# Performance work log

Measured on AMD Instinct MI355X. Metric: run time of the kernel, lower is better.

## Reference

```python
import jax, jax.numpy as jnp
import numpy as np

N, E, D, L = 50000, 640000, 128, 3  # nodes, edges, channels, layers
EPS = 1e-5


def setup_inputs() -> dict:
    key = jax.random.key(0)
    ks = jax.random.split(key, 10)
    s = 1.0 / np.sqrt(D)
    inp = {
        "x": jax.random.normal(ks[0], (N, D), dtype=jnp.float32),
        "edge_attr": jax.random.normal(ks[1], (E, D), dtype=jnp.float32),
        "w_self": jax.random.normal(ks[2], (L, D, D), dtype=jnp.float32) * s,
        "b_self": jnp.zeros((L, D), dtype=jnp.float32),
        "w_in": jax.random.normal(ks[3], (L, D, D), dtype=jnp.float32) * s,
        "b_in": jnp.zeros((L, D), dtype=jnp.float32),
        "w_rel": jax.random.normal(ks[4], (L, D, D), dtype=jnp.float32) * s,
        "b_rel": jnp.zeros((L, D), dtype=jnp.float32),
        "bn_gamma": jnp.ones((L - 1, D), dtype=jnp.float32),
        "bn_beta": jnp.zeros((L - 1, D), dtype=jnp.float32),
        "edge_index": jax.random.randint(ks[5], (2, E), 0, N, dtype=jnp.int64),
    }
    return inp


def _batchnorm(h, gamma, beta):
    mu = jnp.mean(h, axis=0)
    var = jnp.mean(jnp.square(h - mu), axis=0)  # biased var (torch BN training)
    return (h - mu) * jax.lax.rsqrt(var + EPS) * gamma + beta


def reference(x, edge_attr, w_self, b_self, w_in, b_in, w_rel, b_rel,
              bn_gamma, bn_beta, edge_index):
    src, dst = edge_index[0], edge_index[1]
    # per-node in-degree for mean aggregation (zero-degree nodes -> 0)
    cnt = jax.ops.segment_sum(jnp.ones((E, 1), x.dtype), dst, num_segments=N)
    denom = jnp.maximum(cnt, 1.0)
    for i in range(L):
        # message: lin_in(x_j * edge_attr)
        msg = jnp.einsum('ed,fd->ef', x[src] * edge_attr, w_in[i]) + b_in[i]
        agg = jax.ops.segment_sum(msg, dst, num_segments=N) / denom  # scatter-mean
        x = agg + jnp.einsum('nd,fd->nf', x, w_self[i]) + b_self[i]
        edge_attr = jnp.einsum('ed,fd->ef', edge_attr, w_rel[i]) + b_rel[i]
        if i < L - 1:
            x = jax.nn.relu(_batchnorm(x, bn_gamma[i], bn_beta[i]))
            # dropout p=0.0 -> identity
    return (x, edge_attr)
```

## Files before the change

kernel.cpp:

```cpp
#include <hip/hip_runtime.h>

#define DD 128

typedef __attribute__((ext_vector_type(8))) short bf16x8;
typedef __attribute__((ext_vector_type(4))) short bf16x4;
typedef __attribute__((ext_vector_type(4))) float f32x4;
typedef unsigned short u16;

__device__ __forceinline__ unsigned short f2bf(float f) {
  union { float f; unsigned u; } v; v.f = f;
  unsigned u = v.u;
  return (unsigned short)((u + 0x7FFFu + ((u >> 16) & 1u)) >> 16);
}
__device__ __forceinline__ float bf2f(unsigned short h) {
  union { unsigned u; float f; } v; v.u = ((unsigned)h) << 16; return v.f;
}
__device__ __forceinline__ bf16x8 pack8(f32x4 a, f32x4 b) {
  bf16x8 r;
  r[0] = (short)f2bf(a.x); r[1] = (short)f2bf(a.y);
  r[2] = (short)f2bf(a.z); r[3] = (short)f2bf(a.w);
  r[4] = (short)f2bf(b.x); r[5] = (short)f2bf(b.y);
  r[6] = (short)f2bf(b.z); r[7] = (short)f2bf(b.w);
  return r;
}

__device__ __forceinline__ bool idx_is64(const int* p) {
  return (p[1] | p[3] | p[5] | p[7]) == 0;
}
__device__ __forceinline__ int ld_idx(const int* p, long long i, bool is64) {
  return is64 ? (int)((const long long*)p)[i] : p[i];
}

__global__ void k_count(const int* __restrict__ idx, int* __restrict__ cnt, int E) {
  int e = blockIdx.x * blockDim.x + threadIdx.x;
  if (e >= E) return;
  bool is64 = idx_is64(idx);
  int d = ld_idx(idx, (long long)E + e, is64);
  atomicAdd(&cnt[d], 1);
}

__global__ __launch_bounds__(1024) void k_scan(const int* __restrict__ cnt,
    int* __restrict__ row_start, int* __restrict__ cursor, int N) {
  __shared__ int part[1024];
  int t = threadIdx.x;
  int chunk = (N + 1023) >> 10;
  int lo = t * chunk, hi = lo + chunk; if (hi > N) hi = N; if (lo > N) lo = N;
  int s = 0;
  for (int i = lo; i < hi; ++i) s += cnt[i];
  part[t] = s;
  __syncthreads();
  for (int off = 1; off < 1024; off <<= 1) {
    int v = (t >= off) ? part[t - off] : 0;
    __syncthreads();
    part[t] += v;
    __syncthreads();
  }
  int run = (t == 0) ? 0 : part[t - 1];
  for (int i = lo; i < hi; ++i) {
    row_start[i] = run; cursor[i] = run; run += cnt[i];
  }
  if (t == 1023) row_start[N] = part[1023];
}

__global__ void k_fill(const int* __restrict__ idx, int* __restrict__ cursor,
                       int* __restrict__ edge_of, int* __restrict__ src_csr, int E) {
  int e = blockIdx.x * blockDim.x + threadIdx.x;
  if (e >= E) return;
  bool is64 = idx_is64(idx);
  int s = ld_idx(idx, e, is64);
  int d = ld_idx(idx, (long long)E + e, is64);
  int pos = atomicAdd(&cursor[d], 1);
  edge_of[pos] = e;
  src_csr[pos] = s;
}

template <int MODE>
__global__ __launch_bounds__(256) void k_msg(
    const float* __restrict__ x0, const u16* __restrict__ xp,
    const float* __restrict__ ea0, const u16* __restrict__ eain,
    u16* __restrict__ m, u16* __restrict__ eaC,
    const int* __restrict__ edge_of, const int* __restrict__ src_csr, int E) {
  int i = blockIdx.x * 256 + threadIdx.x;
  int k = i >> 4, c = i & 15;
  if (k >= E) return;
  int sn = src_csr[k];
  int co = c * 8;
  bf16x8 mm;
  if constexpr (MODE == 0) {
    int e = edge_of[k];
    const float* ep = ea0 + (size_t)e * DD + co;
    const float* xq = x0 + (size_t)sn * DD + co;
    f32x4 e0 = *(const f32x4*)ep, e1 = *(const f32x4*)(ep + 4);
    f32x4 xv0 = *(const f32x4*)xq, xv1 = *(const f32x4*)(xq + 4);
    *(bf16x8*)(eaC + (size_t)k * DD + co) = pack8(e0, e1);
    f32x4 p0 = e0 * xv0, p1 = e1 * xv1;
    mm = pack8(p0, p1);
  } else {
    bf16x8 ev = *(const bf16x8*)(eain + (size_t)k * DD + co);
    bf16x8 xv = *(const bf16x8*)(xp + (size_t)sn * DD + co);
#pragma unroll
    for (int j = 0; j < 8; ++j)
      mm[j] = (short)f2bf(bf2f((u16)ev[j]) * bf2f((u16)xv[j]));
  }
  *(bf16x8*)(m + (size_t)k * DD + co) = mm;
}

__global__ __launch_bounds__(256) void k_segsum(const u16* __restrict__ m,
    const int* __restrict__ row_start, u16* __restrict__ agg, int N) {
  int n = blockIdx.x * 4 + (threadIdx.x >> 6);
  if (n >= N) return;
  int lane = threadIdx.x & 63;
  int e4 = lane >> 4, c = lane & 15, co = c * 8;
  int s0 = row_start[n], s1 = row_start[n + 1];
  int len = s1 - s0;
  float acc[8];
#pragma unroll
  for (int j = 0; j < 8; ++j) acc[j] = 0.f;
  for (int kk = e4; kk < len; kk += 4) {
    bf16x8 mv = *(const bf16x8*)(m + (size_t)(s0 + kk) * DD + co);
#pragma unroll
    for (int j = 0; j < 8; ++j) acc[j] += bf2f((u16)mv[j]);
  }
#pragma unroll
  for (int j = 0; j < 8; ++j) {
    float s = acc[j];
    s += __shfl_xor(s, 16);
    s += __shfl_xor(s, 32);
    acc[j] = s;
  }
  if (e4 == 0) {
    float inv = (len > 0) ? 1.0f / (float)len : 0.0f;
    f32x4 lo, hi;
#pragma unroll
    for (int j = 0; j < 4; ++j) { lo[j] = acc[j] * inv; hi[j] = acc[4 + j] * inv; }
    *(bf16x8*)(agg + (size_t)n * DD + co) = pack8(lo, hi);
  }
}

template <bool SCATTER, typename TO>
__global__ __launch_bounds__(256, 3) void k_rel(const u16* __restrict__ ea_in,
    TO* __restrict__ ea_out, const int* __restrict__ edge_of,
    const float* __restrict__ W, const float* __restrict__ bias, int ntiles) {
  __shared__ short Wl[16384];
  for (int q = threadIdx.x; q < 4096; q += 256) {
    int off = q * 4;
    int f = off >> 7, d = off & 127;
    f32x4 w = *(const f32x4*)(W + off);
    unsigned byte = ((unsigned)(f * 256 + d * 2)) ^ (unsigned)((f & 7) << 4);
    bf16x4 s4;
    s4[0] = (short)f2bf(w.x); s4[1] = (short)f2bf(w.y);
    s4[2] = (short)f2bf(w.z); s4[3] = (short)f2bf(w.w);
    *(bf16x4*)((char*)Wl + byte) = s4;
  }
  __syncthreads();
  int wave = threadIdx.x >> 6, lane = threadIdx.x & 63;
  int r = lane & 15, g = lane >> 4;
  int tile = blockIdx.x * 4 + wave;
  if (tile >= ntiles) return;
  const u16* rowp = ea_in + (size_t)(tile * 16 + r) * DD;
  bf16x8 a8[4];
#pragma unroll
  for (int ks = 0; ks < 4; ++ks) a8[ks] = *(const bf16x8*)(rowp + ks * 32 + g * 8);
  f32x4 acc[8];
#pragma unroll
  for (int ct = 0; ct < 8; ++ct) acc[ct] = (f32x4){0.f, 0.f, 0.f, 0.f};
#pragma unroll
  for (int ct = 0; ct < 8; ++ct) {
    int f = ct * 16 + r;
    unsigned base = (unsigned)(f * 256);
    unsigned sw = (unsigned)((f & 7) << 4);
#pragma unroll
    for (int ks = 0; ks < 4; ++ks) {
      unsigned byte = (base + (unsigned)(ks * 64 + g * 16)) ^ sw;
      bf16x8 bb = *(const bf16x8*)((const char*)Wl + byte);
      acc[ct] = __builtin_amdgcn_mfma_f32_16x16x32_bf16(a8[ks], bb, acc[ct], 0, 0, 0);
    }
  }
  size_t orow[4];
#pragma unroll
  for (int j = 0; j < 4; ++j) {
    int kr = tile * 16 + g * 4 + j;
    orow[j] = SCATTER ? (size_t)edge_of[kr] : (size_t)kr;
  }
#pragma unroll
  for (int ct = 0; ct < 8; ++ct) {
    int col = ct * 16 + r;
    float bv = bias[col];
#pragma unroll
    for (int j = 0; j < 4; ++j) {
      float v = acc[ct][j] + bv;
      if constexpr (sizeof(TO) == 2) ea_out[orow[j] * DD + col] = (TO)f2bf(v);
      else                            ea_out[orow[j] * DD + col] = (TO)v;
    }
  }
}

template <typename TX, typename TO, bool STATS>
__global__ __launch_bounds__(256, 2) void k_node(const u16* __restrict__ agg,
    const TX* __restrict__ xc, const float* __restrict__ W_in,
    const float* __restrict__ W_self, const float* __restrict__ b_in,
    const float* __restrict__ b_self, const int* __restrict__ row_start,
    TO* __restrict__ xn, float* __restrict__ gsum, float* __restrict__ gssq,
    int ntiles) {
  __shared__ short Wl[DD * 256];
  for (int q = threadIdx.x; q < DD * 256 / 4; q += 256) {
    int off = q * 4;
    int f = off >> 8, k = off & 255;
    f32x4 w = (k < 128) ? *(const f32x4*)(W_in + f * 128 + k)
                        : *(const f32x4*)(W_self + f * 128 + (k - 128));
    unsigned byte = ((unsigned)(f * 512 + k * 2)) ^ (unsigned)((f & 7) << 4);
    bf16x4 s4;
    s4[0] = (short)f2bf(w.x); s4[1] = (short)f2bf(w.y);
    s4[2] = (short)f2bf(w.z); s4[3] = (short)f2bf(w.w);
    *(bf16x4*)((char*)Wl + byte) = s4;
  }
  __syncthreads();
  int wave = threadIdx.x >> 6, lane = threadIdx.x & 63;
  int tile = blockIdx.x * 4 + wave;
  if (tile >= ntiles) return;
  int r = lane & 15, g = lane >> 4;
  int arowi = tile * 16 + r;
  const u16* arow = agg + (size_t)arowi * DD;
  const TX* xrow = xc + (size_t)arowi * DD;
  bf16x8 a[8];
#pragma unroll
  for (int ks = 0; ks < 4; ++ks) a[ks] = *(const bf16x8*)(arow + ks * 32 + g * 8);
#pragma unroll
  for (int ks = 0; ks < 4; ++ks) {
    int c0 = ks * 32 + g * 8;
    if constexpr (sizeof(TX) == 2) {
      a[4 + ks] = *(const bf16x8*)(xrow + c0);
    } else {
      const float* p = (const float*)xrow + c0;
      a[4 + ks] = pack8(*(const f32x4*)p, *(const f32x4*)(p + 4));
    }
  }
  f32x4 acc[8];
#pragma unroll
  for (int ct = 0; ct < 8; ++ct) acc[ct] = (f32x4){0.f, 0.f, 0.f, 0.f};
#pragma unroll
  for (int ct = 0; ct < 8; ++ct) {
    int f = ct * 16 + r;
    unsigned base = (unsigned)(f * 512);
    unsigned sw = (unsigned)((f & 7) << 4);
#pragma unroll
    for (int ks = 0; ks < 8; ++ks) {
      unsigned byte = (base + (unsigned)(ks * 64 + g * 16)) ^ sw;
      bf16x8 b = *(const bf16x8*)((const char*)Wl + byte);
      acc[ct] = __builtin_amdgcn_mfma_f32_16x16x32_bf16(a[ks], b, acc[ct], 0, 0, 0);
    }
  }
  int nbase = tile * 16;
  float degmask[4];
#pragma unroll
  for (int j = 0; j < 4; ++j) {
    int nn = nbase + g * 4 + j;
    degmask[j] = (row_start[nn + 1] > row_start[nn]) ? 1.0f : 0.0f;
  }
#pragma unroll
  for (int ct = 0; ct < 8; ++ct) {
    int col = ct * 16 + r;
    float bi = b_in[col], bs = b_self[col];
    float s = 0.f, s2 = 0.f;
#pragma unroll
    for (int j = 0; j < 4; ++j) {
      float v = acc[ct][j] + bs + bi * degmask[j];
      if constexpr (sizeof(TO) == 2) xn[(size_t)(nbase + g * 4 + j) * DD + col] = (TO)f2bf(v);
      else                            xn[(size_t)(nbase + g * 4 + j) * DD + col] = (TO)v;
      s += v; s2 += v * v;
    }
    if constexpr (STATS) {
      s += __shfl_xor(s, 16);  s += __shfl_xor(s, 32);
      s2 += __shfl_xor(s2, 16); s2 += __shfl_xor(s2, 32);
      if (g == 0) { atomicAdd(&gsum[col], s); atomicAdd(&gssq[col], s2); }
    }
  }
}

__global__ void k_bnfin(float* __restrict__ gsum, float* __restrict__ gssq,
    const float* __restrict__ gamma, const float* __restrict__ beta,
    float* __restrict__ scale, float* __restrict__ shift, int N) {
  int d = threadIdx.x;
  float mu = gsum[d] / (float)N;
  float var = gssq[d] / (float)N - mu * mu;
  float rs = rsqrtf(var + 1e-5f);
  float sc = rs * gamma[d];
  scale[d] = sc;
  shift[d] = beta[d] - mu * sc;
  gsum[d] = 0.f;
  gssq[d] = 0.f;
}

__global__ void k_bnapply(const u16* __restrict__ xb, u16* __restrict__ xpost,
                          const float* __restrict__ scale,
                          const float* __restrict__ shift, int total8) {
  int i = blockIdx.x * blockDim.x + threadIdx.x;
  if (i >= total8) return;
  bf16x8 v = ((const bf16x8*)xb)[i];
  int c0 = (i * 8) & 127;
  bf16x8 o;
#pragma unroll
  for (int j = 0; j < 8; ++j) {
    float f = fmaxf(bf2f((u16)v[j]) * scale[c0 + j] + shift[c0 + j], 0.f);
    o[j] = (short)f2bf(f);
  }
  ((bf16x8*)xpost)[i] = o;
}

static inline size_t alignup(size_t v, size_t a) { return (v + a - 1) & ~(a - 1); }

extern "C" void kernel_launch(void* const* d_in, const int* in_sizes, int n_in,
                              void* d_out, int out_size, void* d_ws, size_t ws_size,
                              hipStream_t stream) {
  const float* x0     = (const float*)d_in[0];
  const float* ea0    = (const float*)d_in[1];
  const float* w_self = (const float*)d_in[2];
  const float* b_self = (const float*)d_in[3];
  const float* w_in   = (const float*)d_in[4];
  const float* b_in   = (const float*)d_in[5];
  const float* w_rel  = (const float*)d_in[6];
  const float* b_rel  = (const float*)d_in[7];
  const float* gamma  = (const float*)d_in[8];
  const float* beta   = (const float*)d_in[9];
  const int*   idx    = (const int*)d_in[10];

  const int N = in_sizes[0] / DD;
  const int E = in_sizes[1] / DD;

  char* w = (char*)d_ws;
  size_t off = 0;
  int* cnt       = (int*)(w + off); off = alignup(off + (size_t)N * 4, 256);
  int* row_start = (int*)(w + off); off = alignup(off + (size_t)(N + 1) * 4, 256);
  int* cursor    = (int*)(w + off); off = alignup(off + (size_t)N * 4, 256);
  int* edge_of   = (int*)(w + off); off = alignup(off + (size_t)E * 4, 256);
  int* src_csr   = (int*)(w + off); off = alignup(off + (size_t)E * 4, 256);
  float* gstats  = (float*)(w + off); off = alignup(off + 256 * 4, 256);
  float* scale   = (float*)(w + off); off = alignup(off + 128 * 4, 256);
  float* shift   = (float*)(w + off); off = alignup(off + 128 * 4, 256);
  u16* agg       = (u16*)(w + off); off = alignup(off + (size_t)N * DD * 2, 256);
  u16* xbA       = (u16*)(w + off); off = alignup(off + (size_t)N * DD * 2, 256);
  u16* xpost     = (u16*)(w + off); off = alignup(off + (size_t)N * DD * 2, 256);
  u16* eaC       = (u16*)(w + off); off = alignup(off + (size_t)E * DD * 2, 256);
  u16* mbuf      = (u16*)(w + off); off = alignup(off + (size_t)E * DD * 2, 256);
  float* gsum = gstats, *gssq = gstats + 128;
  (void)ws_size; (void)n_in; (void)out_size;

  float* out_x  = (float*)d_out;
  float* out_ea = out_x + (size_t)N * DD;

  (void)hipMemsetAsync(cnt, 0, (size_t)N * 4, stream);
  int ethreads = 256, eblocks = (E + ethreads - 1) / ethreads;
  k_count<<<eblocks, ethreads, 0, stream>>>(idx, cnt, E);
  k_scan<<<1, 1024, 0, stream>>>(cnt, row_start, cursor, N);
  k_fill<<<eblocks, ethreads, 0, stream>>>(idx, cursor, edge_of, src_csr, E);
  (void)hipMemsetAsync(gstats, 0, 256 * 4, stream);

  const int ntN = N / 16;
  const int ntE = E / 16;
  const int msgBlocks = (E * 16 + 255) / 256;
  const int segBlocks = (N + 3) / 4;
  const int relBlocks = (ntE + 3) / 4;
  const int nodeBlocks = (ntN + 3) / 4;
  const int bnBlocks = ((size_t)N * DD / 8 + 255) / 256;

  k_msg<0><<<msgBlocks, 256, 0, stream>>>(x0, nullptr, ea0, nullptr,
      mbuf, eaC, edge_of, src_csr, E);
  k_rel<false, u16><<<relBlocks, 256, 0, stream>>>(eaC, eaC, edge_of,
      w_rel, b_rel, ntE);
  k_segsum<<<segBlocks, 256, 0, stream>>>(mbuf, row_start, agg, N);
  k_node<float, u16, true><<<nodeBlocks, 256, 0, stream>>>(agg, x0,
      w_in, w_self, b_in, b_self, row_start, xbA, gsum, gssq, ntN);
  k_bnfin<<<1, 128, 0, stream>>>(gsum, gssq, gamma, beta, scale, shift, N);
  k_bnapply<<<bnBlocks, 256, 0, stream>>>(xbA, xpost, scale, shift, N * DD / 8);

  k_msg<1><<<msgBlocks, 256, 0, stream>>>(nullptr, xpost, nullptr, eaC,
      mbuf, nullptr, edge_of, src_csr, E);
  k_rel<false, u16><<<relBlocks, 256, 0, stream>>>(eaC, eaC, edge_of,
      w_rel + DD * DD, b_rel + DD, ntE);
  k_segsum<<<segBlocks, 256, 0, stream>>>(mbuf, row_start, agg, N);
  k_node<u16, u16, true><<<nodeBlocks, 256, 0, stream>>>(agg, xpost,
      w_in + DD * DD, w_self + DD * DD, b_in + DD, b_self + DD,
      row_start, xbA, gsum, gssq, ntN);
  k_bnfin<<<1, 128, 0, stream>>>(gsum, gssq, gamma + DD, beta + DD, scale, shift, N);
  k_bnapply<<<bnBlocks, 256, 0, stream>>>(xbA, xpost, scale, shift, N * DD / 8);

  k_msg<1><<<msgBlocks, 256, 0, stream>>>(nullptr, xpost, nullptr, eaC,
      mbuf, nullptr, edge_of, src_csr, E);
  k_rel<true, float><<<relBlocks, 256, 0, stream>>>(eaC, out_ea, edge_of,
      w_rel + 2 * DD * DD, b_rel + 2 * DD, ntE);
  k_segsum<<<segBlocks, 256, 0, stream>>>(mbuf, row_start, agg, N);
  k_node<u16, float, false><<<nodeBlocks, 256, 0, stream>>>(agg, xpost,
      w_in + 2 * DD * DD, w_self + 2 * DD * DD, b_in + 2 * DD, b_self + 2 * DD,
      row_start, out_x, gsum, gssq, ntN);
}
```

Measured before the change: 1.215 ms.

## Fuse message, edge-linear and batchnorm-apply into combined edge and node kernels

Merges the per-edge message kernel and the edge relation GEMM into one k_relmsg kernel, so each edge tile reads edge_attr once and writes both the message and the transformed edge features. It also drops the separate batchnorm-apply pass by applying scale, shift and ReLU on the fly when the message and node kernels read node features. This removes several full passes over E×D and N×D buffers and some kernel launches. In exchange, it double-buffers edge features because input and output rows no longer align within one kernel, it adds register pressure (launch bound 2 instead of 3), and BN+ReLU is now recomputed on every gathered source row.

```diff
diff --git a/kernel.cpp b/kernel.cpp
--- a/kernel.cpp
+++ b/kernel.cpp
@@ -75,34 +75,128 @@
 }
 
 template <int MODE>
-__global__ __launch_bounds__(256) void k_msg(
-    const float* __restrict__ x0, const u16* __restrict__ xp,
+__global__ __launch_bounds__(256, 2) void k_relmsg(
+    const float* __restrict__ x0, const u16* __restrict__ xbin,
     const float* __restrict__ ea0, const u16* __restrict__ eain,
-    u16* __restrict__ m, u16* __restrict__ eaC,
-    const int* __restrict__ edge_of, const int* __restrict__ src_csr, int E) {
-  int i = blockIdx.x * 256 + threadIdx.x;
-  int k = i >> 4, c = i & 15;
-  if (k >= E) return;
-  int sn = src_csr[k];
-  int co = c * 8;
-  bf16x8 mm;
+    u16* __restrict__ eabout, float* __restrict__ eafout,
+    u16* __restrict__ m,
+    const int* __restrict__ edge_of, const int* __restrict__ src_csr,
+    const float* __restrict__ w_rel, const float* __restrict__ b_rel,
+    const float* __restrict__ scale, const float* __restrict__ shift,
+    int ntE) {
+  __shared__ short Wl[16384];
+  for (int q = threadIdx.x; q < 4096; q += 256) {
+    int off = q * 4;
+    int f = off >> 7, d = off & 127;
+    f32x4 w = *(const f32x4*)(w_rel + off);
+    unsigned byte = ((unsigned)(f * 256 + d * 2)) ^ (unsigned)((f & 7) << 4);
+    bf16x4 s4;
+    s4[0] = (short)f2bf(w.x); s4[1] = (short)f2bf(w.y);
+    s4[2] = (short)f2bf(w.z); s4[3] = (short)f2bf(w.w);
+    *(bf16x4*)((char*)Wl + byte) = s4;
+  }
+  __syncthreads();
+  int wave = threadIdx.x >> 6, lane = threadIdx.x & 63;
+  int tile = blockIdx.x * 4 + wave;
+  if (tile >= ntE) return;
+  int r = lane & 15, g = lane >> 4;
+  int k0 = tile * 16;
+  int pos = r;
+  int co = pos * 8;
+
+  bf16x8 a8[4];
   if constexpr (MODE == 0) {
-    int e = edge_of[k];
-    const float* ep = ea0 + (size_t)e * DD + co;
-    const float* xq = x0 + (size_t)sn * DD + co;
-    f32x4 e0 = *(const f32x4*)ep, e1 = *(const f32x4*)(ep + 4);
-    f32x4 xv0 = *(const f32x4*)xq, xv1 = *(const f32x4*)(xq + 4);
-    *(bf16x8*)(eaC + (size_t)k * DD + co) = pack8(e0, e1);
-    f32x4 p0 = e0 * xv0, p1 = e1 * xv1;
-    mm = pack8(p0, p1);
+    int er = edge_of[k0 + r];
+    const float* rp = ea0 + (size_t)er * DD;
+#pragma unroll
+    for (int ks = 0; ks < 4; ++ks) {
+      const float* p = rp + ks * 32 + g * 8;
+      a8[ks] = pack8(*(const f32x4*)p, *(const f32x4*)(p + 4));
+    }
   } else {
-    bf16x8 ev = *(const bf16x8*)(eain + (size_t)k * DD + co);
-    bf16x8 xv = *(const bf16x8*)(xp + (size_t)sn * DD + co);
-#pragma unroll
-    for (int j = 0; j < 8; ++j)
-      mm[j] = (short)f2bf(bf2f((u16)ev[j]) * bf2f((u16)xv[j]));
-  }
-  *(bf16x8*)(m + (size_t)k * DD + co) = mm;
+    const u16* rp = eain + (size_t)(k0 + r) * DD;
+#pragma unroll
+    for (int ks = 0; ks < 4; ++ks) a8[ks] = *(const bf16x8*)(rp + ks * 32 + g * 8);
+  }
+
+  int kk[4], sn[4];
+#pragma unroll
+  for (int i = 0; i < 4; ++i) { kk[i] = k0 + g + 4 * i; sn[i] = src_csr[kk[i]]; }
+  f32x4 xf0[4], xf1[4], ef0[4], ef1[4];
+  bf16x8 xb[4], eb[4];
+  if constexpr (MODE == 0) {
+#pragma unroll
+    for (int i = 0; i < 4; ++i) {
+      int ei = edge_of[kk[i]];
+      const float* xp = x0 + (size_t)sn[i] * DD + co;
+      const float* ep = ea0 + (size_t)ei * DD + co;
+      xf0[i] = *(const f32x4*)xp; xf1[i] = *(const f32x4*)(xp + 4);
+      ef0[i] = *(const f32x4*)ep; ef1[i] = *(const f32x4*)(ep + 4);
+    }
+  } else {
+#pragma unroll
+    for (int i = 0; i < 4; ++i) {
+      xb[i] = *(const bf16x8*)(xbin + (size_t)sn[i] * DD + co);
+      eb[i] = *(const bf16x8*)(eain + (size_t)kk[i] * DD + co);
+    }
+  }
+  float sc[8], sh[8];
+  if constexpr (MODE >= 1) {
+    f32x4 s0 = *(const f32x4*)(scale + co), s1 = *(const f32x4*)(scale + co + 4);
+    f32x4 h0 = *(const f32x4*)(shift + co), h1 = *(const f32x4*)(shift + co + 4);
+#pragma unroll
+    for (int j = 0; j < 4; ++j) { sc[j] = s0[j]; sc[4 + j] = s1[j]; sh[j] = h0[j]; sh[4 + j] = h1[j]; }
+  }
+
+  f32x4 acc[8];
+#pragma unroll
+  for (int ct = 0; ct < 8; ++ct) acc[ct] = (f32x4){0.f, 0.f, 0.f, 0.f};
+#pragma unroll
+  for (int ct = 0; ct < 8; ++ct) {
+    int f = ct * 16 + r;
+    unsigned base = (unsigned)(f * 256);
+    unsigned sw = (unsigned)((f & 7) << 4);
+#pragma unroll
+    for (int ks = 0; ks < 4; ++ks) {
+      unsigned byte = (base + (unsigned)(ks * 64 + g * 16)) ^ sw;
+      bf16x8 bb = *(const bf16x8*)((const char*)Wl + byte);
+      acc[ct] = __builtin_amdgcn_mfma_f32_16x16x32_bf16(a8[ks], bb, acc[ct], 0, 0, 0);
+    }
+  }
+
+#pragma unroll
+  for (int i = 0; i < 4; ++i) {
+    bf16x8 mm;
+    if constexpr (MODE == 0) {
+      f32x4 p0 = xf0[i] * ef0[i], p1 = xf1[i] * ef1[i];
+      mm = pack8(p0, p1);
+    } else {
+#pragma unroll
+      for (int j = 0; j < 8; ++j) {
+        float xv = fmaxf(bf2f((u16)xb[i][j]) * sc[j] + sh[j], 0.f);
+        mm[j] = (short)f2bf(xv * bf2f((u16)eb[i][j]));
+      }
+    }
+    *(bf16x8*)(m + (size_t)kk[i] * DD + co) = mm;
+  }
+
+  size_t orow[4];
+#pragma unroll
+  for (int j = 0; j < 4; ++j) {
+    int kr = k0 + g * 4 + j;
+    orow[j] = (MODE == 2) ? (size_t)edge_of[kr] : (size_t)kr;
+  }
+#pragma unroll
+  for (int ct = 0; ct < 8; ++ct) {
+    int col = ct * 16 + r;
+    float bv = b_rel[col];
+#pragma unroll
+    for (int j = 0; j < 4; ++j) {
+      float v = acc[ct][j] + bv;
+      if constexpr (MODE == 2) eafout[orow[j] * DD + col] = v;
+      else                     eabout[orow[j] * DD + col] = f2bf(v);
+    }
+  }
 }
 
 __global__ __launch_bounds__(256) void k_segsum(const u16* __restrict__ m,
@@ -137,69 +231,12 @@
   }
 }
 
-template <bool SCATTER, typename TO>
-__global__ __launch_bounds__(256, 3) void k_rel(const u16* __restrict__ ea_in,
-    TO* __restrict__ ea_out, const int* __restrict__ edge_of,
-    const float* __restrict__ W, const float* __restrict__ bias, int ntiles) {
-  __shared__ short Wl[16384];
-  for (int q = threadIdx.x; q < 4096; q += 256) {
-    int off = q * 4;
-    int f = off >> 7, d = off & 127;
-    f32x4 w = *(const f32x4*)(W + off);
-    unsigned byte = ((unsigned)(f * 256 + d * 2)) ^ (unsigned)((f & 7) << 4);
-    bf16x4 s4;
-    s4[0] = (short)f2bf(w.x); s4[1] = (short)f2bf(w.y);
-    s4[2] = (short)f2bf(w.z); s4[3] = (short)f2bf(w.w);
-    *(bf16x4*)((char*)Wl + byte) = s4;
-  }
-  __syncthreads();
-  int wave = threadIdx.x >> 6, lane = threadIdx.x & 63;
-  int r = lane & 15, g = lane >> 4;
-  int tile = blockIdx.x * 4 + wave;
-  if (tile >= ntiles) return;
-  const u16* rowp = ea_in + (size_t)(tile * 16 + r) * DD;
-  bf16x8 a8[4];
-#pragma unroll
-  for (int ks = 0; ks < 4; ++ks) a8[ks] = *(const bf16x8*)(rowp + ks * 32 + g * 8);
-  f32x4 acc[8];
-#pragma unroll
-  for (int ct = 0; ct < 8; ++ct) acc[ct] = (f32x4){0.f, 0.f, 0.f, 0.f};
-#pragma unroll
-  for (int ct = 0; ct < 8; ++ct) {
-    int f = ct * 16 + r;
-    unsigned base = (unsigned)(f * 256);
-    unsigned sw = (unsigned)((f & 7) << 4);
-#pragma unroll
-    for (int ks = 0; ks < 4; ++ks) {
-      unsigned byte = (base + (unsigned)(ks * 64 + g * 16)) ^ sw;
-      bf16x8 bb = *(const bf16x8*)((const char*)Wl + byte);
-      acc[ct] = __builtin_amdgcn_mfma_f32_16x16x32_bf16(a8[ks], bb, acc[ct], 0, 0, 0);
-    }
-  }
-  size_t orow[4];
-#pragma unroll
-  for (int j = 0; j < 4; ++j) {
-    int kr = tile * 16 + g * 4 + j;
-    orow[j] = SCATTER ? (size_t)edge_of[kr] : (size_t)kr;
-  }
-#pragma unroll
-  for (int ct = 0; ct < 8; ++ct) {
-    int col = ct * 16 + r;
-    float bv = bias[col];
-#pragma unroll
-    for (int j = 0; j < 4; ++j) {
-      float v = acc[ct][j] + bv;
-      if constexpr (sizeof(TO) == 2) ea_out[orow[j] * DD + col] = (TO)f2bf(v);
-      else                            ea_out[orow[j] * DD + col] = (TO)v;
-    }
-  }
-}
-
-template <typename TX, typename TO, bool STATS>
+template <typename TX, bool BN, typename TO, bool STATS>
 __global__ __launch_bounds__(256, 2) void k_node(const u16* __restrict__ agg,
     const TX* __restrict__ xc, const float* __restrict__ W_in,
     const float* __restrict__ W_self, const float* __restrict__ b_in,
     const float* __restrict__ b_self, const int* __restrict__ row_start,
+    const float* __restrict__ scale, const float* __restrict__ shift,
     TO* __restrict__ xn, float* __restrict__ gsum, float* __restrict__ gssq,
     int ntiles) {
   __shared__ short Wl[DD * 256];
@@ -229,7 +266,18 @@
   for (int ks = 0; ks < 4; ++ks) {
     int c0 = ks * 32 + g * 8;
     if constexpr (sizeof(TX) == 2) {
-      a[4 + ks] = *(const bf16x8*)(xrow + c0);
+      bf16x8 raw = *(const bf16x8*)(xrow + c0);
+      if constexpr (BN) {
+        bf16x8 fr;
+#pragma unroll
+        for (int j = 0; j < 8; ++j) {
+          float f = fmaxf(bf2f((u16)raw[j]) * scale[c0 + j] + shift[c0 + j], 0.f);
+          fr[j] = (short)f2bf(f);
+        }
+        a[4 + ks] = fr;
+      } else {
+        a[4 + ks] = raw;
+      }
     } else {
       const float* p = (const float*)xrow + c0;
       a[4 + ks] = pack8(*(const f32x4*)p, *(const f32x4*)(p + 4));
@@ -289,22 +337,6 @@
   shift[d] = beta[d] - mu * sc;
   gsum[d] = 0.f;
   gssq[d] = 0.f;
-}
-
-__global__ void k_bnapply(const u16* __restrict__ xb, u16* __restrict__ xpost,
-                          const float* __restrict__ scale,
-                          const float* __restrict__ shift, int total8) {
-  int i = blockIdx.x * blockDim.x + threadIdx.x;
-  if (i >= total8) return;
-  bf16x8 v = ((const bf16x8*)xb)[i];
-  int c0 = (i * 8) & 127;
-  bf16x8 o;
-#pragma unroll
-  for (int j = 0; j < 8; ++j) {
-    float f = fmaxf(bf2f((u16)v[j]) * scale[c0 + j] + shift[c0 + j], 0.f);
-    o[j] = (short)f2bf(f);
-  }
-  ((bf16x8*)xpost)[i] = o;
 }
 
 static inline size_t alignup(size_t v, size_t a) { return (v + a - 1) & ~(a - 1); }
@@ -339,8 +371,9 @@
   float* shift   = (float*)(w + off); off = alignup(off + 128 * 4, 256);
   u16* agg       = (u16*)(w + off); off = alignup(off + (size_t)N * DD * 2, 256);
   u16* xbA       = (u16*)(w + off); off = alignup(off + (size_t)N * DD * 2, 256);
-  u16* xpost     = (u16*)(w + off); off = alignup(off + (size_t)N * DD * 2, 256);
-  u16* eaC       = (u16*)(w + off); off = alignup(off + (size_t)E * DD * 2, 256);
+  u16* xbB       = (u16*)(w + off); off = alignup(off + (size_t)N * DD * 2, 256);
+  u16* eaA       = (u16*)(w + off); off = alignup(off + (size_t)E * DD * 2, 256);
+  u16* eaB       = (u16*)(w + off); off = alignup(off + (size_t)E * DD * 2, 256);
   u16* mbuf      = (u16*)(w + off); off = alignup(off + (size_t)E * DD * 2, 256);
   float* gsum = gstats, *gssq = gstats + 128;
   (void)ws_size; (void)n_in; (void)out_size;
@@ -357,39 +390,31 @@
 
   const int ntN = N / 16;
   const int ntE = E / 16;
-  const int msgBlocks = (E * 16 + 255) / 256;
+  const int rmBlocks = (ntE + 3) / 4;
   const int segBlocks = (N + 3) / 4;
-  const int relBlocks = (ntE + 3) / 4;
   const int nodeBlocks = (ntN + 3) / 4;
-  const int bnBlocks = ((size_t)N * DD / 8 + 255) / 256;
-
-  k_msg<0><<<msgBlocks, 256, 0, stream>>>(x0, nullptr, ea0, nullptr,
-      mbuf, eaC, edge_of, src_csr, E);
-  k_rel<false, u16><<<relBlocks, 256, 0, stream>>>(eaC, eaC, edge_of,
-      w_rel, b_rel, ntE);
+
+  k_relmsg<0><<<rmBlocks, 256, 0, stream>>>(x0, nullptr, ea0, nullptr,
+      eaA, nullptr, mbuf, edge_of, src_csr, w_rel, b_rel, scale, shift, ntE);
   k_segsum<<<segBlocks, 256, 0, stream>>>(mbuf, row_start, agg, N);
-  k_node<float, u16, true><<<nodeBlocks, 256, 0, stream>>>(agg, x0,
-      w_in, w_self, b_in, b_self, row_start, xbA, gsum, gssq, ntN);
+  k_node<float, false, u16, true><<<nodeBlocks, 256, 0, stream>>>(agg, x0,
+      w_in, w_self, b_in, b_self, row_start, scale, shift, xbA, gsum, gssq, ntN);
   k_bnfin<<<1, 128, 0, stream>>>(gsum, gssq, gamma, beta, scale, shift, N);
-  k_bnapply<<<bnBlocks, 256, 0, stream>>>(xbA, xpost, scale, shift, N * DD / 8);
-
-  k_msg<1><<<msgBlocks, 256, 0, stream>>>(nullptr, xpost, nullptr, eaC,
-      mbuf, nullptr, edge_of, src_csr, E);
-  k_rel<false, u16><<<relBlocks, 256, 0, stream>>>(eaC, eaC, edge_of,
-      w_rel + DD * DD, b_rel + DD, ntE);
+
+  k_relmsg<1><<<rmBlocks, 256, 0, stream>>>(nullptr, xbA, nullptr, eaA,
+      eaB, nullptr, mbuf, edge_of, src_csr,
+      w_rel + DD * DD, b_rel + DD, scale, shift, ntE);
   k_segsum<<<segBlocks, 256, 0, stream>>>(mbuf, row_start, agg, N);
-  k_node<u16, u16, true><<<nodeBlocks, 256, 0, stream>>>(agg, xpost,
+  k_node<u16, true, u16, true><<<nodeBlocks, 256, 0, stream>>>(agg, xbA,
       w_in + DD * DD, w_self + DD * DD, b_in + DD, b_self + DD,
-      row_start, xbA, gsum, gssq, ntN);
+      row_start, scale, shift, xbB, gsum, gssq, ntN);
   k_bnfin<<<1, 128, 0, stream>>>(gsum, gssq, gamma + DD, beta + DD, scale, shift, N);
-  k_bnapply<<<bnBlocks, 256, 0, stream>>>(xbA, xpost, scale, shift, N * DD / 8);
-
-  k_msg<1><<<msgBlocks, 256, 0, stream>>>(nullptr, xpost, nullptr, eaC,
-      mbuf, nullptr, edge_of, src_csr, E);
-  k_rel<true, float><<<relBlocks, 256, 0, stream>>>(eaC, out_ea, edge_of,
-      w_rel + 2 * DD * DD, b_rel + 2 * DD, ntE);
+
+  k_relmsg<2><<<rmBlocks, 256, 0, stream>>>(nullptr, xbB, nullptr, eaB,
+      nullptr, out_ea, mbuf, edge_of, src_csr,
+      w_rel + 2 * DD * DD, b_rel + 2 * DD, scale, shift, ntE);
   k_segsum<<<segBlocks, 256, 0, stream>>>(mbuf, row_start, agg, N);
-  k_node<u16, float, false><<<nodeBlocks, 256, 0, stream>>>(agg, xpost,
+  k_node<u16, true, float, false><<<nodeBlocks, 256, 0, stream>>>(agg, xbB,
       w_in + 2 * DD * DD, w_self + 2 * DD * DD, b_in + 2 * DD, b_self + 2 * DD,
-      row_start, out_x, gsum, gssq, ntN);
-}
+      row_start, scale, shift, out_x, gsum, gssq, ntN);
+}
```

Result: faster. 1.136 ms (-6.5%).
